# Optimization experiments

Measured on AMD Instinct MI355X. Metric: run time of the kernel, lower is better.

Reference implementation:

```python
import jax, jax.numpy as jnp
import numpy as np
from jax import lax

B, T, N, D = 8, 64, 197, 768
HID = 4
K_FRAME, K_TOKEN = 8, 49
LAMBDA_COV, LAMBDA_SCORE = 1.0, 0.5
LN_EPS = 1e-5


def setup_inputs() -> dict:
    key = jax.random.key(0)
    k = jax.random.split(key, 5)
    x = jax.random.normal(k[0], (B, T, N, D), jnp.float32)
    mask = jax.random.uniform(k[1], (B, T, N), jnp.float32)
    ln_gamma = jnp.ones((D,), jnp.float32)
    ln_beta = jnp.zeros((D,), jnp.float32)
    W1 = jax.random.normal(k[2], (D, HID * D), jnp.float32) * 0.02
    b1 = jnp.zeros((HID * D,), jnp.float32)
    W2 = jax.random.normal(k[3], (HID * D, 1), jnp.float32) * 0.02
    b2 = jnp.zeros((1,), jnp.float32)
    return {"x": x, "mask": mask, "ln_gamma": ln_gamma, "ln_beta": ln_beta,
            "W1": W1, "b1": b1, "W2": W2, "b2": b2}


def _facility_location(frame_repr, score, valid, k):
    # cosine similarity between frames (F.normalize eps = 1e-12)
    fn = frame_repr / jnp.clip(jnp.linalg.norm(frame_repr, axis=-1, keepdims=True), 1e-12)
    sim = jnp.einsum('bid,bjd->bij', fn, fn)  # [B,T,T]
    Bb, Tt = score.shape

    def step(carry, _):
        best_cover, chosen = carry  # [B,T], [B,T] bool
        # coverage gain per candidate j: sum_i max(best[i], sim[i,j]) - best[i]
        cov_gain = jnp.maximum(best_cover[:, :, None], sim).sum(1) - best_cover.sum(1, keepdims=True)
        total = LAMBDA_COV * cov_gain + LAMBDA_SCORE * score
        total = jnp.where(valid & (~chosen), total, -jnp.inf)
        j = jnp.argmax(total, axis=1)  # [B]
        sim_j = jnp.take_along_axis(sim, j[:, None, None], axis=2)[..., 0]  # [B,T]
        best_cover = jnp.maximum(best_cover, sim_j)
        chosen = chosen.at[jnp.arange(Bb), j].set(True)
        return (best_cover, chosen), j

    init = (jnp.zeros((Bb, Tt), frame_repr.dtype), jnp.zeros((Bb, Tt), bool))
    (_, chosen), js = lax.scan(step, init, None, length=k)
    return js.T, chosen.astype(frame_repr.dtype)  # frame_idx [B,k], frame_mask [B,T]


def _kcenter(X, valid, k):
    # X [N,D], valid [N] bool; greedy k-center (farthest point sampling)
    d0 = jnp.where(valid, (X * X).sum(-1), -jnp.inf)
    first = jnp.argmax(d0)

    def dist_to(i):
        diff = X - X[i]
        return jnp.sqrt((diff * diff).sum(-1))

    min_dist = jnp.where(valid, dist_to(first), -1.0)

    def step(md, _):
        cand = jnp.argmax(md)
        md = jnp.where(valid, jnp.minimum(md, dist_to(cand)), -1.0)
        return md, cand

    _, rest = lax.scan(step, min_dist, None, length=k - 1)
    return jnp.concatenate([first[None], rest])


def _forward(x, mask, ln_gamma, ln_beta, W1, b1, W2, b2):
    # masked mean frame representation (use_cls=False path)
    denom = jnp.clip(mask.sum(2), 1e-6)                      # [B,T]
    frame_repr = (x * mask[..., None]).sum(2) / denom[..., None]  # [B,T,D]
    valid_frame = denom > 0

    # score head: LayerNorm -> Linear -> GELU(exact) -> Linear
    mu = frame_repr.mean(-1, keepdims=True)
    var = ((frame_repr - mu) ** 2).mean(-1, keepdims=True)
    h = (frame_repr - mu) / jnp.sqrt(var + LN_EPS) * ln_gamma + ln_beta
    h = jax.nn.gelu(h @ W1 + b1, approximate=False)
    score = (h @ W2 + b2)[..., 0]                            # [B,T]

    # selection is index-valued: no gradient flows through it (as in torch)
    frame_idx, frame_mask = _facility_location(
        lax.stop_gradient(frame_repr), lax.stop_gradient(score), valid_frame, K_FRAME)

    Xf = jnp.take_along_axis(x, frame_idx[:, :, None, None], axis=1)   # [B,K,N,D]
    mf = jnp.take_along_axis(mask, frame_idx[:, :, None], axis=1) > 0.5  # [B,K,N]

    token_idx = jax.vmap(jax.vmap(lambda Xs, vs: _kcenter(Xs, vs, K_TOKEN)))(
        lax.stop_gradient(Xf), mf)                           # [B,K,Kt]

    b_ar = jnp.arange(x.shape[0])
    token_mask = jnp.zeros(mask.shape, x.dtype).at[
        b_ar[:, None, None], frame_idx[:, :, None], token_idx].set(1.0)

    z = jnp.take_along_axis(Xf, token_idx[..., None], axis=2)  # [B,K,Kt,D]
    return z, frame_idx, token_idx, frame_mask, token_mask


def reference(x, mask, ln_gamma, ln_beta, W1, b1, W2, b2):
    return _forward(x, mask, ln_gamma, ln_beta, W1, b1, W2, b2)
```

## Files before the change

kernel.cpp:

```cpp
#include <hip/hip_runtime.h>
#include <math.h>

#define B_ 8
#define T_ 64
#define N_ 197
#define D_ 768
#define HIDD_ 3072
#define KF_ 8
#define KT_ 49
#define GSTRIDE 200

#define Z_SZ    (B_*KF_*KT_*D_)
#define FI_OFF  (Z_SZ)
#define TI_OFF  (FI_OFF + B_*KF_)
#define FM_OFF  (TI_OFF + B_*KF_*KT_)
#define TM_OFF  (FM_OFF + B_*T_)
#define TM_SZ   (B_*T_*N_)

#define WS_SCOREP  0
#define WS_FN64    98304
#define WS_H32     (WS_FN64 + 3145728)
#define WS_VALID   (WS_H32 + 1572864)
#define WS_FIDX    (WS_VALID + 2048)
#define WS_TOK     (WS_FIDX + 256)
#define WS_G       (WS_TOK + 12800)

__global__ __launch_bounds__(256) void kA(const float* __restrict__ x,
                                          const float* __restrict__ mask,
                                          const float* __restrict__ gamma,
                                          const float* __restrict__ beta,
                                          double* __restrict__ fn64,
                                          float* __restrict__ h32,
                                          int* __restrict__ validw) {
  const int row = blockIdx.x;
  const int tid = threadIdx.x;
  __shared__ float  ms[N_];
  __shared__ double red[256];
  __shared__ double sh_denom, sh_mu, sh_sd, sh_nrm;
  const float* xr = x + (size_t)row * (N_ * D_);

  if (tid < N_) ms[tid] = mask[(size_t)row * N_ + tid];
  __syncthreads();

  red[tid] = (tid < N_) ? (double)ms[tid] : 0.0;
  __syncthreads();
  for (int s = 128; s > 0; s >>= 1) { if (tid < s) red[tid] += red[tid + s]; __syncthreads(); }
  if (tid == 0) { double d = red[0]; sh_denom = (d > 1e-6) ? d : 1e-6; }
  __syncthreads();
  const double dn = sh_denom;

  double a0 = 0.0, a1 = 0.0, a2 = 0.0, a3 = 0.0;
  if (tid < 192) {
    const float* px = xr + tid * 4;
#pragma unroll 4
    for (int n = 0; n < N_; n++) {
      const double mv = (double)ms[n];
      const float4 v = *(const float4*)(px + (size_t)n * D_);
      a0 += (double)v.x * mv;
      a1 += (double)v.y * mv;
      a2 += (double)v.z * mv;
      a3 += (double)v.w * mv;
    }
  }
  const double f0 = a0 / dn, f1 = a1 / dn, f2 = a2 / dn, f3 = a3 / dn;

  red[tid] = (tid < 192) ? (f0 + f1 + f2 + f3) : 0.0; __syncthreads();
  for (int s = 128; s > 0; s >>= 1) { if (tid < s) red[tid] += red[tid + s]; __syncthreads(); }
  if (tid == 0) sh_mu = red[0] / (double)D_;
  __syncthreads();
  const double mu = sh_mu;

  red[tid] = (tid < 192) ? (f0 * f0 + f1 * f1 + f2 * f2 + f3 * f3) : 0.0; __syncthreads();
  for (int s = 128; s > 0; s >>= 1) { if (tid < s) red[tid] += red[tid + s]; __syncthreads(); }
  if (tid == 0) { double nr = sqrt(red[0]); sh_nrm = (nr > 1e-12) ? nr : 1e-12; }
  __syncthreads();

  red[tid] = (tid < 192) ? ((f0 - mu) * (f0 - mu) + (f1 - mu) * (f1 - mu) +
                            (f2 - mu) * (f2 - mu) + (f3 - mu) * (f3 - mu)) : 0.0;
  __syncthreads();
  for (int s = 128; s > 0; s >>= 1) { if (tid < s) red[tid] += red[tid + s]; __syncthreads(); }
  if (tid == 0) sh_sd = sqrt(red[0] / (double)D_ + 1e-5);
  __syncthreads();
  const double sd = sh_sd, nrm = sh_nrm;

  if (tid < 192) {
    const size_t base = (size_t)row * D_;
    const float4 g  = ((const float4*)gamma)[tid];
    const float4 be = ((const float4*)beta)[tid];
    float4 hv;
    hv.x = (float)((f0 - mu) / sd * (double)g.x + (double)be.x);
    hv.y = (float)((f1 - mu) / sd * (double)g.y + (double)be.y);
    hv.z = (float)((f2 - mu) / sd * (double)g.z + (double)be.z);
    hv.w = (float)((f3 - mu) / sd * (double)g.w + (double)be.w);
    *(float4*)(h32 + base + tid * 4) = hv;
    double2* fp = (double2*)(fn64 + base + tid * 4);
    fp[0] = make_double2(f0 / nrm, f1 / nrm);
    fp[1] = make_double2(f2 / nrm, f3 / nrm);
  }
  if (tid == 0) validw[row] = 1;
}

__global__ __launch_bounds__(256) void kB(const float* __restrict__ h32,
                                          const float* __restrict__ W1,
                                          const float* __restrict__ b1,
                                          const float* __restrict__ W2,
                                          double* __restrict__ scorep) {
  const int n0 = blockIdx.x * 128;
  const int m0 = blockIdx.y * 32;
  const int tid = threadIdx.x;
  const int tx = tid & 31;
  const int ty = tid >> 5;
  __shared__ float As[64 * 33];
  __shared__ float Bs[64 * 128];
  float acc[4][4];
#pragma unroll
  for (int r = 0; r < 4; r++)
#pragma unroll
    for (int c = 0; c < 4; c++) acc[r][c] = 0.0f;

  for (int kc = 0; kc < 12; kc++) {
    const int k0 = kc * 64;
#pragma unroll
    for (int it = 0; it < 8; it++) {
      int idx = tid + (it << 8);
      int k = idx & 63, m = idx >> 6;
      As[k * 33 + m] = h32[(size_t)(m0 + m) * D_ + k0 + k];
    }
#pragma unroll
    for (int it = 0; it < 8; it++) {
      int idx = tid + (it << 8);
      int k = idx >> 5, n4 = idx & 31;
      const float4 v = *(const float4*)(W1 + (size_t)(k0 + k) * HIDD_ + n0 + (n4 << 2));
      *(float4*)(Bs + k * 128 + (n4 << 2)) = v;
    }
    __syncthreads();
#pragma unroll 16
    for (int kk = 0; kk < 64; kk++) {
      float a[4], bb[4];
#pragma unroll
      for (int r = 0; r < 4; r++) a[r] = As[kk * 33 + ty * 4 + r];
#pragma unroll
      for (int c = 0; c < 4; c++) bb[c] = Bs[kk * 128 + tx * 4 + c];
#pragma unroll
      for (int r = 0; r < 4; r++)
#pragma unroll
        for (int c = 0; c < 4; c++) acc[r][c] += a[r] * bb[c];
    }
    __syncthreads();
  }

  double part[4] = {0.0, 0.0, 0.0, 0.0};
#pragma unroll
  for (int r = 0; r < 4; r++) {
#pragma unroll
    for (int c = 0; c < 4; c++) {
      const int gn = n0 + tx * 4 + c;
      const double v = (double)(acc[r][c] + b1[gn]);
      const double g = 0.5 * v * (1.0 + erf(v * 0.7071067811865475244));
      part[r] += g * (double)W2[gn];
    }
  }
#pragma unroll
  for (int r = 0; r < 4; r++) {
    double s = part[r];
#pragma unroll
    for (int off = 16; off > 0; off >>= 1) s += __shfl_down(s, off, 32);
    if (tx == 0) scorep[(size_t)(m0 + ty * 4 + r) * 24 + blockIdx.x] = s;
  }
}

__global__ __launch_bounds__(256) void kD(const double* __restrict__ fn64,
                                          const double* __restrict__ scorep,
                                          const int* __restrict__ validw,
                                          const float* __restrict__ b2,
                                          int* __restrict__ fidxw,
                                          float* __restrict__ out_fidx,
                                          float* __restrict__ out_fmask) {
  const int b = blockIdx.x;
  const int tid = threadIdx.x;
  __shared__ double fnS[64 * 65];
  __shared__ double sim[64 * 64];
  __shared__ double scoreS[64];
  __shared__ double bc[64];
  __shared__ int chosenS[64];
  __shared__ int validS[64];

  const int i0 = (tid >> 4) << 2;
  const int j0 = (tid & 15) << 2;
  double acc[4][4];
#pragma unroll
  for (int r = 0; r < 4; r++)
#pragma unroll
    for (int c = 0; c < 4; c++) acc[r][c] = 0.0;

  for (int c = 0; c < 12; c++) {
#pragma unroll
    for (int it = 0; it < 16; it++) {
      int idx = (it << 8) + tid;
      int t = idx >> 6, kk = idx & 63;
      fnS[t * 65 + kk] = fn64[((size_t)(b * T_ + t)) * D_ + c * 64 + kk];
    }
    __syncthreads();
#pragma unroll 4
    for (int kk = 0; kk < 64; kk++) {
      double a[4], bb[4];
#pragma unroll
      for (int r = 0; r < 4; r++) a[r] = fnS[(i0 + r) * 65 + kk];
#pragma unroll
      for (int cc = 0; cc < 4; cc++) bb[cc] = fnS[(j0 + cc) * 65 + kk];
#pragma unroll
      for (int r = 0; r < 4; r++)
#pragma unroll
        for (int cc = 0; cc < 4; cc++) acc[r][cc] += a[r] * bb[cc];
    }
    __syncthreads();
  }
#pragma unroll
  for (int r = 0; r < 4; r++)
#pragma unroll
    for (int cc = 0; cc < 4; cc++) sim[(i0 + r) * 64 + (j0 + cc)] = acc[r][cc];

  if (tid < 64) {
    double s = 0.0;
    const double* sp = scorep + (size_t)(b * T_ + tid) * 24;
    for (int q = 0; q < 24; q++) s += sp[q];
    scoreS[tid]  = s + (double)b2[0];
    validS[tid]  = validw[b * T_ + tid];
    bc[tid]      = 0.0;
    chosenS[tid] = 0;
  }
  __syncthreads();

  for (int step = 0; step < KF_; step++) {
    if (tid < 64) {
      double g = 0.0;
      for (int ii = 0; ii < 64; ii++) g += fmax(bc[ii], sim[ii * 64 + tid]);
      double bs = bc[tid];
#pragma unroll
      for (int off = 32; off > 0; off >>= 1) bs += __shfl_down(bs, off, 64);
      bs = __shfl(bs, 0, 64);
      double tot = g - bs + 0.5 * scoreS[tid];
      if (!validS[tid] || chosenS[tid]) tot = -INFINITY;
      double bv = tot; int bi = tid;
#pragma unroll
      for (int off = 32; off > 0; off >>= 1) {
        double ov = __shfl_down(bv, off, 64);
        int    oi = __shfl_down(bi, off, 64);
        if (ov > bv || (ov == bv && oi < bi)) { bv = ov; bi = oi; }
      }
      bi = __shfl(bi, 0, 64);
      bc[tid] = fmax(bc[tid], sim[tid * 64 + bi]);
      if (tid == bi) chosenS[tid] = 1;
      if (tid == 0) {
        fidxw[b * KF_ + step] = bi;
        out_fidx[b * KF_ + step] = (float)bi;
      }
    }
    __syncthreads();
  }
  if (tid < 64) out_fmask[b * T_ + tid] = chosenS[tid] ? 1.0f : 0.0f;
}

__global__ __launch_bounds__(256) void kG(const float* __restrict__ x,
                                          const int* __restrict__ fidxw,
                                          double* __restrict__ G) {
  static const int TIa[10] = {0,0,0,0,1,1,1,2,2,3};
  static const int TJa[10] = {0,1,2,3,1,2,3,2,3,3};
  const int p  = blockIdx.x / 10;
  const int t  = blockIdx.x - p * 10;
  const int ti = TIa[t], tj = TJa[t];
  const int b  = p >> 3;
  const int fi = fidxw[p];
  const float* X = x + ((size_t)(b * T_ + fi)) * (N_ * D_);
  double* Gp = G + (size_t)p * (GSTRIDE * GSTRIDE);

  __shared__ double As[32 * 65];
  __shared__ double Bs[32 * 65];
  const int tid = threadIdx.x;
  const int tx = tid & 15;
  const int ty = tid >> 4;
  double acc[4][4];
#pragma unroll
  for (int r = 0; r < 4; r++)
#pragma unroll
    for (int c = 0; c < 4; c++) acc[r][c] = 0.0;

  for (int kc = 0; kc < 24; kc++) {
#pragma unroll
    for (int it = 0; it < 2; it++) {
      const int idx = (it << 8) + tid;
      const int row = idx >> 3;
      const int kg  = idx & 7;
      const int gra = ti * 64 + row, grb = tj * 64 + row;
      const int ra = (gra < N_) ? gra : (N_ - 1);
      const int rb = (grb < N_) ? grb : (N_ - 1);
      const float4 va = *(const float4*)(X + (size_t)ra * D_ + kc * 32 + kg * 4);
      const float4 vb = *(const float4*)(X + (size_t)rb * D_ + kc * 32 + kg * 4);
      As[(kg * 4 + 0) * 65 + row] = (double)va.x;
      As[(kg * 4 + 1) * 65 + row] = (double)va.y;
      As[(kg * 4 + 2) * 65 + row] = (double)va.z;
      As[(kg * 4 + 3) * 65 + row] = (double)va.w;
      Bs[(kg * 4 + 0) * 65 + row] = (double)vb.x;
      Bs[(kg * 4 + 1) * 65 + row] = (double)vb.y;
      Bs[(kg * 4 + 2) * 65 + row] = (double)vb.z;
      Bs[(kg * 4 + 3) * 65 + row] = (double)vb.w;
    }
    __syncthreads();
#pragma unroll 8
    for (int kk = 0; kk < 32; kk++) {
      double a[4], bb[4];
#pragma unroll
      for (int q = 0; q < 4; q++) a[q]  = As[kk * 65 + ty + 16 * q];
#pragma unroll
      for (int q = 0; q < 4; q++) bb[q] = Bs[kk * 65 + tx + 16 * q];
#pragma unroll
      for (int r = 0; r < 4; r++)
#pragma unroll
        for (int c = 0; c < 4; c++) acc[r][c] += a[r] * bb[c];
    }
    __syncthreads();
  }

#pragma unroll
  for (int r = 0; r < 4; r++) {
    const int gi = ti * 64 + ty + 16 * r;
#pragma unroll
    for (int c = 0; c < 4; c++) {
      const int gj = tj * 64 + tx + 16 * c;
      if (gi < N_ && gj < N_) {
        Gp[(size_t)gi * GSTRIDE + gj] = acc[r][c];
        if (ti != tj) Gp[(size_t)gj * GSTRIDE + gi] = acc[r][c];
      }
    }
  }
}

__global__ __launch_bounds__(256) void kE2(const double* __restrict__ G,
                                           const float* __restrict__ mask,
                                           const int* __restrict__ fidxw,
                                           int* __restrict__ tokw) {
  const int p = blockIdx.x;
  const int b = p >> 3;
  const int fi = fidxw[p];
  const double* Gp = G + (size_t)p * (GSTRIDE * GSTRIDE);
  const float* mrow = mask + (size_t)(b * T_ + fi) * N_;
  const int tid = threadIdx.x;
  const bool live = tid < N_;

  __shared__ double gds[N_];
  __shared__ double bvS[4];
  __shared__ int biS[4];
  __shared__ int candS;

  const int valid = (live && mrow[tid] > 0.5f) ? 1 : 0;
  const double gd = live ? Gp[(size_t)tid * GSTRIDE + tid] : 0.0;
  if (live) gds[tid] = gd;
  __syncthreads();

  auto argmax = [&](double v) -> int {
    double bv = v; int bi = tid;
#pragma unroll
    for (int off = 32; off > 0; off >>= 1) {
      const double ov = __shfl_down(bv, off, 64);
      const int    oi = __shfl_down(bi, off, 64);
      if (ov > bv || (ov == bv && oi < bi)) { bv = ov; bi = oi; }
    }
    const int w = tid >> 6;
    if ((tid & 63) == 0) { bvS[w] = bv; biS[w] = bi; }
    __syncthreads();
    if (tid == 0) {
      double B0 = bvS[0]; int best = biS[0];
      for (int q = 1; q < 4; q++)
        if (bvS[q] > B0) { B0 = bvS[q]; best = biS[q]; }
      candS = best;
    }
    __syncthreads();
    return candS;
  };

  int cand = argmax((live && valid) ? gd : -INFINITY);
  if (tid == 0) tokw[p * KT_] = cand;

  double md = -INFINITY;
  for (int k = 1; k < KT_; k++) {
    const double gdc = gds[cand];
    const double g = live ? Gp[(size_t)cand * GSTRIDE + tid] : 0.0;
    const double dist = sqrt(fmax(gd + gdc - 2.0 * g, 0.0));
    if (live) md = valid ? ((k == 1) ? dist : fmin(md, dist)) : -1.0;
    cand = argmax(md);
    if (tid == 0) tokw[p * KT_ + k] = cand;
  }
}

__global__ __launch_bounds__(256) void kF(const float* __restrict__ x,
                                          const int* __restrict__ fidxw,
                                          const int* __restrict__ tokw,
                                          float* __restrict__ out) {
  const int row = blockIdx.x * 4 + (threadIdx.x >> 6);
  const int lane = threadIdx.x & 63;
  const int pair = row / KT_;
  const int b = pair >> 3;
  const int fi = fidxw[pair];
  const int tok = tokw[row];
  const float* src = x + (((size_t)(b * T_ + fi)) * N_ + tok) * D_;
  float* dst = out + (size_t)row * D_;
#pragma unroll
  for (int r = 0; r < 3; r++) {
    const int d = lane * 4 + 256 * r;
    *(float4*)(dst + d) = *(const float4*)(src + d);
  }
  if (lane == 0) {
    out[TI_OFF + row] = (float)tok;
    out[TM_OFF + (size_t)(b * T_ + fi) * N_ + tok] = 1.0f;
  }
}

extern "C" void kernel_launch(void* const* d_in, const int* in_sizes, int n_in,
                              void* d_out, int out_size, void* d_ws, size_t ws_size,
                              hipStream_t stream) {
  (void)in_sizes; (void)n_in; (void)ws_size; (void)out_size;
  const float* x     = (const float*)d_in[0];
  const float* mask  = (const float*)d_in[1];
  const float* gamma = (const float*)d_in[2];
  const float* beta  = (const float*)d_in[3];
  const float* W1    = (const float*)d_in[4];
  const float* b1    = (const float*)d_in[5];
  const float* W2    = (const float*)d_in[6];
  const float* b2    = (const float*)d_in[7];
  float* out = (float*)d_out;
  char* ws = (char*)d_ws;

  double* scorep = (double*)(ws + WS_SCOREP);
  double* fn64   = (double*)(ws + WS_FN64);
  float*  h32    = (float*)(ws + WS_H32);
  int*    validw = (int*)(ws + WS_VALID);
  int*    fidxw  = (int*)(ws + WS_FIDX);
  int*    tokw   = (int*)(ws + WS_TOK);
  double* G      = (double*)(ws + WS_G);

  hipMemsetAsync(out + TM_OFF, 0, (size_t)TM_SZ * sizeof(float), stream);

  kA<<<B_ * T_, 256, 0, stream>>>(x, mask, gamma, beta, fn64, h32, validw);
  kB<<<dim3(HIDD_ / 128, (B_ * T_) / 32), 256, 0, stream>>>(h32, W1, b1, W2, scorep);
  kD<<<B_, 256, 0, stream>>>(fn64, scorep, validw, b2, fidxw, out + FI_OFF, out + FM_OFF);
  kG<<<B_ * KF_ * 10, 256, 0, stream>>>(x, fidxw, G);
  kE2<<<B_ * KF_, 256, 0, stream>>>(G, mask, fidxw, tokw);
  kF<<<B_ * KF_ * KT_ / 4, 256, 0, stream>>>(x, fidxw, tokw, out);
}
```

Measured before the change: 833.3 us.

## Split frame similarity into separate kernel, vectorize GEMM LDS reads, fuse gather into k-center

```diff
diff --git a/kernel.cpp b/kernel.cpp
--- a/kernel.cpp
+++ b/kernel.cpp
@@ -22,8 +22,8 @@
 #define WS_H32     (WS_FN64 + 3145728)
 #define WS_VALID   (WS_H32 + 1572864)
 #define WS_FIDX    (WS_VALID + 2048)
-#define WS_TOK     (WS_FIDX + 256)
-#define WS_G       (WS_TOK + 12800)
+#define WS_SIM     (WS_FIDX + 256)
+#define WS_G       (WS_SIM + 262144)
 
 __global__ __launch_bounds__(256) void kA(const float* __restrict__ x,
                                           const float* __restrict__ mask,
@@ -110,7 +110,7 @@
   const int tid = threadIdx.x;
   const int tx = tid & 31;
   const int ty = tid >> 5;
-  __shared__ float As[64 * 33];
+  __shared__ float As[64 * 36];
   __shared__ float Bs[64 * 128];
   float acc[4][4];
 #pragma unroll
@@ -124,7 +124,7 @@
     for (int it = 0; it < 8; it++) {
       int idx = tid + (it << 8);
       int k = idx & 63, m = idx >> 6;
-      As[k * 33 + m] = h32[(size_t)(m0 + m) * D_ + k0 + k];
+      As[k * 36 + m] = h32[(size_t)(m0 + m) * D_ + k0 + k];
     }
 #pragma unroll
     for (int it = 0; it < 8; it++) {
@@ -136,11 +136,10 @@
     __syncthreads();
 #pragma unroll 16
     for (int kk = 0; kk < 64; kk++) {
-      float a[4], bb[4];
-#pragma unroll
-      for (int r = 0; r < 4; r++) a[r] = As[kk * 33 + ty * 4 + r];
-#pragma unroll
-      for (int c = 0; c < 4; c++) bb[c] = Bs[kk * 128 + tx * 4 + c];
+      float4 av = *(const float4*)(As + kk * 36 + ty * 4);
+      float4 bv = *(const float4*)(Bs + kk * 128 + tx * 4);
+      const float a[4] = {av.x, av.y, av.z, av.w};
+      const float bb[4] = {bv.x, bv.y, bv.z, bv.w};
 #pragma unroll
       for (int r = 0; r < 4; r++)
 #pragma unroll
@@ -169,7 +168,47 @@
   }
 }
 
-__global__ __launch_bounds__(256) void kD(const double* __restrict__ fn64,
+__global__ __launch_bounds__(256) void kS(const double* __restrict__ fn64,
+                                          double* __restrict__ simG) {
+  const int b    = blockIdx.x >> 2;
+  const int tile = blockIdx.x & 3;
+  const int tid = threadIdx.x;
+  const int ty = tid >> 4;
+  const int tx = tid & 15;
+  __shared__ double As[64 * 17];
+  __shared__ double Bs[64 * 66];
+  double acc[4] = {0.0, 0.0, 0.0, 0.0};
+
+  for (int kc = 0; kc < 12; kc++) {
+#pragma unroll
+    for (int it = 0; it < 4; it++) {
+      const int idx = (it << 8) + tid;
+      const int row = idx >> 6, kk = idx & 63;
+      As[kk * 17 + row] = fn64[((size_t)(b * T_ + tile * 16 + row)) * D_ + kc * 64 + kk];
+    }
+#pragma unroll
+    for (int it = 0; it < 16; it++) {
+      const int idx = (it << 8) + tid;
+      const int row = idx >> 6, kk = idx & 63;
+      Bs[kk * 66 + row] = fn64[((size_t)(b * T_ + row)) * D_ + kc * 64 + kk];
+    }
+    __syncthreads();
+#pragma unroll 8
+    for (int kk = 0; kk < 64; kk++) {
+      const double a = As[kk * 17 + ty];
+      const double* bp = Bs + kk * 66 + tx * 4;
+      acc[0] += a * bp[0];
+      acc[1] += a * bp[1];
+      acc[2] += a * bp[2];
+      acc[3] += a * bp[3];
+    }
+    __syncthreads();
+  }
+  double* o = simG + ((size_t)b * 64 + tile * 16 + ty) * 64 + tx * 4;
+  o[0] = acc[0]; o[1] = acc[1]; o[2] = acc[2]; o[3] = acc[3];
+}
+
+__global__ __launch_bounds__(256) void kD(const double* __restrict__ simG,
                                           const double* __restrict__ scorep,
                                           const int* __restrict__ validw,
                                           const float* __restrict__ b2,
@@ -178,52 +217,22 @@
                                           float* __restrict__ out_fmask) {
   const int b = blockIdx.x;
   const int tid = threadIdx.x;
-  __shared__ double fnS[64 * 65];
   __shared__ double sim[64 * 64];
   __shared__ double scoreS[64];
   __shared__ double bc[64];
   __shared__ int chosenS[64];
   __shared__ int validS[64];
 
-  const int i0 = (tid >> 4) << 2;
-  const int j0 = (tid & 15) << 2;
-  double acc[4][4];
-#pragma unroll
-  for (int r = 0; r < 4; r++)
-#pragma unroll
-    for (int c = 0; c < 4; c++) acc[r][c] = 0.0;
-
-  for (int c = 0; c < 12; c++) {
-#pragma unroll
-    for (int it = 0; it < 16; it++) {
-      int idx = (it << 8) + tid;
-      int t = idx >> 6, kk = idx & 63;
-      fnS[t * 65 + kk] = fn64[((size_t)(b * T_ + t)) * D_ + c * 64 + kk];
-    }
-    __syncthreads();
-#pragma unroll 4
-    for (int kk = 0; kk < 64; kk++) {
-      double a[4], bb[4];
-#pragma unroll
-      for (int r = 0; r < 4; r++) a[r] = fnS[(i0 + r) * 65 + kk];
-#pragma unroll
-      for (int cc = 0; cc < 4; cc++) bb[cc] = fnS[(j0 + cc) * 65 + kk];
-#pragma unroll
-      for (int r = 0; r < 4; r++)
-#pragma unroll
-        for (int cc = 0; cc < 4; cc++) acc[r][cc] += a[r] * bb[cc];
-    }
-    __syncthreads();
-  }
-#pragma unroll
-  for (int r = 0; r < 4; r++)
-#pragma unroll
-    for (int cc = 0; cc < 4; cc++) sim[(i0 + r) * 64 + (j0 + cc)] = acc[r][cc];
-
+  const double2* sp = (const double2*)(simG + (size_t)b * 4096);
+#pragma unroll
+  for (int it = 0; it < 8; it++) {
+    const int idx = (it << 8) + tid;
+    ((double2*)sim)[idx] = sp[idx];
+  }
   if (tid < 64) {
     double s = 0.0;
-    const double* sp = scorep + (size_t)(b * T_ + tid) * 24;
-    for (int q = 0; q < 24; q++) s += sp[q];
+    const double* pp = scorep + (size_t)(b * T_ + tid) * 24;
+    for (int q = 0; q < 24; q++) s += pp[q];
     scoreS[tid]  = s + (double)b2[0];
     validS[tid]  = validw[b * T_ + tid];
     bc[tid]      = 0.0;
@@ -274,8 +283,8 @@
   const float* X = x + ((size_t)(b * T_ + fi)) * (N_ * D_);
   double* Gp = G + (size_t)p * (GSTRIDE * GSTRIDE);
 
-  __shared__ double As[32 * 65];
-  __shared__ double Bs[32 * 65];
+  __shared__ float As[32 * 68];
+  __shared__ float Bs[32 * 68];
   const int tid = threadIdx.x;
   const int tx = tid & 15;
   const int ty = tid >> 4;
@@ -296,23 +305,22 @@
       const int rb = (grb < N_) ? grb : (N_ - 1);
       const float4 va = *(const float4*)(X + (size_t)ra * D_ + kc * 32 + kg * 4);
       const float4 vb = *(const float4*)(X + (size_t)rb * D_ + kc * 32 + kg * 4);
-      As[(kg * 4 + 0) * 65 + row] = (double)va.x;
-      As[(kg * 4 + 1) * 65 + row] = (double)va.y;
-      As[(kg * 4 + 2) * 65 + row] = (double)va.z;
-      As[(kg * 4 + 3) * 65 + row] = (double)va.w;
-      Bs[(kg * 4 + 0) * 65 + row] = (double)vb.x;
-      Bs[(kg * 4 + 1) * 65 + row] = (double)vb.y;
-      Bs[(kg * 4 + 2) * 65 + row] = (double)vb.z;
-      Bs[(kg * 4 + 3) * 65 + row] = (double)vb.w;
+      As[(kg * 4 + 0) * 68 + row] = va.x;
+      As[(kg * 4 + 1) * 68 + row] = va.y;
+      As[(kg * 4 + 2) * 68 + row] = va.z;
+      As[(kg * 4 + 3) * 68 + row] = va.w;
+      Bs[(kg * 4 + 0) * 68 + row] = vb.x;
+      Bs[(kg * 4 + 1) * 68 + row] = vb.y;
+      Bs[(kg * 4 + 2) * 68 + row] = vb.z;
+      Bs[(kg * 4 + 3) * 68 + row] = vb.w;
     }
     __syncthreads();
 #pragma unroll 8
     for (int kk = 0; kk < 32; kk++) {
-      double a[4], bb[4];
-#pragma unroll
-      for (int q = 0; q < 4; q++) a[q]  = As[kk * 65 + ty + 16 * q];
-#pragma unroll
-      for (int q = 0; q < 4; q++) bb[q] = Bs[kk * 65 + tx + 16 * q];
+      const float4 av = *(const float4*)(As + kk * 68 + ty * 4);
+      const float4 bv = *(const float4*)(Bs + kk * 68 + tx * 4);
+      const double a[4]  = {(double)av.x, (double)av.y, (double)av.z, (double)av.w};
+      const double bb[4] = {(double)bv.x, (double)bv.y, (double)bv.z, (double)bv.w};
 #pragma unroll
       for (int r = 0; r < 4; r++)
 #pragma unroll
@@ -323,10 +331,10 @@
 
 #pragma unroll
   for (int r = 0; r < 4; r++) {
-    const int gi = ti * 64 + ty + 16 * r;
+    const int gi = ti * 64 + ty * 4 + r;
 #pragma unroll
     for (int c = 0; c < 4; c++) {
-      const int gj = tj * 64 + tx + 16 * c;
+      const int gj = tj * 64 + tx * 4 + c;
       if (gi < N_ && gj < N_) {
         Gp[(size_t)gi * GSTRIDE + gj] = acc[r][c];
         if (ti != tj) Gp[(size_t)gj * GSTRIDE + gi] = acc[r][c];
@@ -338,12 +346,14 @@
 __global__ __launch_bounds__(256) void kE2(const double* __restrict__ G,
                                            const float* __restrict__ mask,
                                            const int* __restrict__ fidxw,
-                                           int* __restrict__ tokw) {
+                                           const float* __restrict__ x,
+                                           float* __restrict__ out) {
   const int p = blockIdx.x;
   const int b = p >> 3;
   const int fi = fidxw[p];
   const double* Gp = G + (size_t)p * (GSTRIDE * GSTRIDE);
   const float* mrow = mask + (size_t)(b * T_ + fi) * N_;
+  const float* X = x + ((size_t)(b * T_ + fi)) * (N_ * D_);
   const int tid = threadIdx.x;
   const bool live = tid < N_;
 
@@ -351,6 +361,7 @@
   __shared__ double bvS[4];
   __shared__ int biS[4];
   __shared__ int candS;
+  __shared__ int toksS[KT_];
 
   const int valid = (live && mrow[tid] > 0.5f) ? 1 : 0;
   const double gd = live ? Gp[(size_t)tid * GSTRIDE + tid] : 0.0;
@@ -379,7 +390,7 @@
   };
 
   int cand = argmax((live && valid) ? gd : -INFINITY);
-  if (tid == 0) tokw[p * KT_] = cand;
+  if (tid == 0) toksS[0] = cand;
 
   double md = -INFINITY;
   for (int k = 1; k < KT_; k++) {
@@ -388,30 +399,20 @@
     const double dist = sqrt(fmax(gd + gdc - 2.0 * g, 0.0));
     if (live) md = valid ? ((k == 1) ? dist : fmin(md, dist)) : -1.0;
     cand = argmax(md);
-    if (tid == 0) tokw[p * KT_ + k] = cand;
-  }
-}
-
-__global__ __launch_bounds__(256) void kF(const float* __restrict__ x,
-                                          const int* __restrict__ fidxw,
-                                          const int* __restrict__ tokw,
-                                          float* __restrict__ out) {
-  const int row = blockIdx.x * 4 + (threadIdx.x >> 6);
-  const int lane = threadIdx.x & 63;
-  const int pair = row / KT_;
-  const int b = pair >> 3;
-  const int fi = fidxw[pair];
-  const int tok = tokw[row];
-  const float* src = x + (((size_t)(b * T_ + fi)) * N_ + tok) * D_;
-  float* dst = out + (size_t)row * D_;
-#pragma unroll
-  for (int r = 0; r < 3; r++) {
-    const int d = lane * 4 + 256 * r;
-    *(float4*)(dst + d) = *(const float4*)(src + d);
-  }
-  if (lane == 0) {
-    out[TI_OFF + row] = (float)tok;
+    if (tid == 0) toksS[k] = cand;
+  }
+  __syncthreads();
+
+  if (tid < KT_) {
+    const int tok = toksS[tid];
+    out[TI_OFF + p * KT_ + tid] = (float)tok;
     out[TM_OFF + (size_t)(b * T_ + fi) * N_ + tok] = 1.0f;
+  }
+  if (tid < 192) {
+    for (int r = 0; r < KT_; r++) {
+      const float4 v = *(const float4*)(X + (size_t)toksS[r] * D_ + tid * 4);
+      *(float4*)(out + ((size_t)(p * KT_ + r)) * D_ + tid * 4) = v;
+    }
   }
 }
 
@@ -435,15 +436,15 @@
   float*  h32    = (float*)(ws + WS_H32);
   int*    validw = (int*)(ws + WS_VALID);
   int*    fidxw  = (int*)(ws + WS_FIDX);
-  int*    tokw   = (int*)(ws + WS_TOK);
+  double* simG   = (double*)(ws + WS_SIM);
   double* G      = (double*)(ws + WS_G);
 
   hipMemsetAsync(out + TM_OFF, 0, (size_t)TM_SZ * sizeof(float), stream);
 
   kA<<<B_ * T_, 256, 0, stream>>>(x, mask, gamma, beta, fn64, h32, validw);
+  kS<<<B_ * 4, 256, 0, stream>>>(fn64, simG);
   kB<<<dim3(HIDD_ / 128, (B_ * T_) / 32), 256, 0, stream>>>(h32, W1, b1, W2, scorep);
-  kD<<<B_, 256, 0, stream>>>(fn64, scorep, validw, b2, fidxw, out + FI_OFF, out + FM_OFF);
+  kD<<<B_, 256, 0, stream>>>(simG, scorep, validw, b2, fidxw, out + FI_OFF, out + FM_OFF);
   kG<<<B_ * KF_ * 10, 256, 0, stream>>>(x, fidxw, G);
-  kE2<<<B_ * KF_, 256, 0, stream>>>(G, mask, fidxw, tokw);
-  kF<<<B_ * KF_ * KT_ / 4, 256, 0, stream>>>(x, fidxw, tokw, out);
-}
+  kE2<<<B_ * KF_, 256, 0, stream>>>(G, mask, fidxw, x, out);
+}
```

Measured after the change: 764.3 us. -8.3%, faster.
